# Optimization experiments

Hardware: AMD Instinct MI355X
Metric: run time of the kernel (lower is better)

## Reference

```python
import jax, jax.numpy as jnp
import numpy as np

IN_CHS = 128
NUM_HEADS = 4
WIN = 7
N = WIN * WIN            # 49 tokens per window
QKDIM = 128              # ceil(in_chs/num_groups/num_heads)*num_heads
HEAD_DIM = QKDIM // NUM_HEADS
SCALE = HEAD_DIM ** -0.5
B = 4096                 # batch * num_windows


def _relative_position_index(win_h, win_w):
    coords = np.stack(np.meshgrid(np.arange(win_h), np.arange(win_w), indexing='ij'))  # [2,h,w]
    cf = coords.reshape(2, -1)                      # [2, N]
    rc = (cf[:, :, None] - cf[:, None, :]).transpose(1, 2, 0).astype(np.int64)  # [N,N,2]
    rc[:, :, 0] += win_h - 1
    rc[:, :, 1] += win_w - 1
    rc[:, :, 0] *= 2 * win_w - 1
    return rc.sum(-1)                               # [N, N]


def setup_inputs() -> dict:
    key = jax.random.key(0)
    ks = jax.random.split(key, 8)
    x = jax.random.normal(ks[0], (B, N, IN_CHS), dtype=jnp.float32)
    qk_w = jax.random.normal(ks[1], (2 * QKDIM, IN_CHS), dtype=jnp.float32) * 0.02
    qk_b = jnp.zeros((2 * QKDIM,), dtype=jnp.float32)
    v_w = jax.random.normal(ks[2], (IN_CHS, IN_CHS), dtype=jnp.float32) * 0.02
    v_b = jnp.zeros((IN_CHS,), dtype=jnp.float32)
    proj_w = jax.random.normal(ks[3], (IN_CHS, IN_CHS), dtype=jnp.float32) * 0.02
    proj_b = jnp.zeros((IN_CHS,), dtype=jnp.float32)
    bias_table = jax.random.normal(ks[4], ((2 * WIN - 1) * (2 * WIN - 1), NUM_HEADS), dtype=jnp.float32) * 0.02
    rel_idx = jnp.asarray(_relative_position_index(WIN, WIN))  # [N,N] int64
    return {"x": x, "qk_w": qk_w, "qk_b": qk_b, "v_w": v_w, "v_b": v_b,
            "proj_w": proj_w, "proj_b": proj_b, "bias_table": bias_table,
            "rel_idx": rel_idx}


def reference(x, qk_w, qk_b, v_w, v_b, proj_w, proj_b, bias_table, rel_idx):
    Bn, Nn, C = x.shape
    # fused q/k projection: [B,N,2*qkdim] -> q,k each [B,H,N,d]
    qk = (x @ qk_w.T + qk_b).reshape(Bn, Nn, 2, NUM_HEADS, HEAD_DIM)
    q = qk[:, :, 0].transpose(0, 2, 1, 3)
    k = qk[:, :, 1].transpose(0, 2, 1, 3)
    v = (x @ v_w.T + v_b).reshape(Bn, Nn, NUM_HEADS, -1).transpose(0, 2, 1, 3)
    # windowed QK^T with gathered relative-position bias
    attn = jnp.einsum('bhnd,bhmd->bhnm', q * SCALE, k)
    bias = bias_table[rel_idx.reshape(-1)].reshape(Nn, Nn, NUM_HEADS).transpose(2, 0, 1)
    attn = jax.nn.softmax(attn + bias[None], axis=-1)
    out = jnp.einsum('bhnm,bhmd->bhnd', attn, v).transpose(0, 2, 1, 3).reshape(Bn, Nn, -1)
    return out @ proj_w.T + proj_b
```

## Files before the change

### kernel.cpp

```cpp
#include <hip/hip_runtime.h>
#include <hip/hip_bf16.h>

typedef __attribute__((ext_vector_type(8))) __bf16 bf16x8;
typedef __attribute__((ext_vector_type(4))) short short4v;
typedef __attribute__((ext_vector_type(4))) float f32x4;

#define MFMA(a,b,c) __builtin_amdgcn_mfma_f32_16x16x32_bf16((a),(b),(c),0,0,0)
#define MFMA16(a,b,c) __builtin_amdgcn_mfma_f32_16x16x16bf16_1k((a),(b),(c),0,0,0)

#define XB 0u
#define QB 16384u
#define KB 32768u
#define VT 49152u

static __device__ __forceinline__ unsigned short f2u(float x) {
  return __builtin_bit_cast(unsigned short, static_cast<__bf16>(x));
}
static __device__ __forceinline__ unsigned long long pack4(float a, float b, float c, float d) {
  union { __bf16 h[4]; unsigned long long u; } z;
  z.h[0] = static_cast<__bf16>(a);
  z.h[1] = static_cast<__bf16>(b);
  z.h[2] = static_cast<__bf16>(c);
  z.h[3] = static_cast<__bf16>(d);
  return z.u;
}
static __device__ __forceinline__ unsigned long long pack4v(f32x4 v) {
  return pack4(v[0], v[1], v[2], v[3]);
}
static __device__ __forceinline__ short4v pack4s(float a, float b, float c, float d) {
  union { __bf16 h[4]; short4v s; } z;
  z.h[0] = static_cast<__bf16>(a);
  z.h[1] = static_cast<__bf16>(b);
  z.h[2] = static_cast<__bf16>(c);
  z.h[3] = static_cast<__bf16>(d);
  return z.s;
}
static __device__ __forceinline__ unsigned sw256(unsigned row, unsigned colb) {
  return (row << 8) + (colb ^ ((row & 7u) << 4));
}
static __device__ __forceinline__ unsigned sw128(unsigned row, unsigned colb) {
  return (row << 7) + (colb ^ ((row & 7u) << 4));
}

__global__ void rsa_prep(const float* __restrict__ qk_w, const float* __restrict__ v_w,
                         const float* __restrict__ proj_w, const float* __restrict__ bias_table,
                         unsigned short* __restrict__ wqk, unsigned short* __restrict__ wv,
                         unsigned short* __restrict__ wp, float* __restrict__ biasNN) {
  const float QSCALE = 0.17677669529663687f * 1.4426950408889634f;
  const float LOG2E = 1.4426950408889634f;
  int t = blockIdx.x * blockDim.x + threadIdx.x;
  int stride = gridDim.x * blockDim.x;
  for (int i = t; i < 256 * 128; i += stride) {
    float v = qk_w[i];
    if (i < 128 * 128) v *= QSCALE;
    wqk[i] = f2u(v);
  }
  for (int i = t; i < 128 * 128; i += stride) wv[i] = f2u(v_w[i]);
  for (int i = t; i < 128 * 128; i += stride) wp[i] = f2u(proj_w[i]);
  for (int i = t; i < 4 * 64 * 64; i += stride) {
    int h = i >> 12, r = (i >> 6) & 63, m = i & 63;
    float v = -1e9f;
    if (r < 49 && m < 49) {
      int ri = r / 7, rj = r - ri * 7, mi = m / 7, mj = m - mi * 7;
      int rel = (ri - mi + 6) * 13 + (rj - mj + 6);
      v = bias_table[rel * 4 + h];
    }
    biasNN[i] = v * LOG2E;
  }
}

__global__ __launch_bounds__(256, 2) void rsa_main(
    const float* __restrict__ x, const float* __restrict__ qk_bias,
    const float* __restrict__ v_bias, const float* __restrict__ proj_bias,
    const unsigned short* __restrict__ wqk, const unsigned short* __restrict__ wv,
    const unsigned short* __restrict__ wp, const float* __restrict__ biasNN,
    float* __restrict__ out) {
  __shared__ __align__(16) unsigned char LDS[65536];
  const int tid = threadIdx.x;
  const int w = tid >> 6;
  const int lane = tid & 63;
  const int c = lane & 15;
  const int g = lane >> 4;
  const int b = blockIdx.x;
  const float QBSCALE = 0.17677669529663687f * 1.4426950408889634f;

  {
    const f32x4* xp = reinterpret_cast<const f32x4*>(x + (size_t)b * 6272);
    for (int i = tid; i < 1568; i += 256) {
      f32x4 v = xp[i];
      unsigned row = (unsigned)i >> 5, c4 = (unsigned)i & 31u;
      *reinterpret_cast<unsigned long long*>(LDS + XB + sw256(row, c4 * 8)) = pack4v(v);
    }
    for (int i = tid; i < 480; i += 256) {
      unsigned row = 49 + ((unsigned)i >> 5), c4 = (unsigned)i & 31u;
      *reinterpret_cast<unsigned long long*>(LDS + XB + sw256(row, c4 * 8)) = 0ull;
    }
  }
  __syncthreads();

  __builtin_amdgcn_s_setprio(1);
#pragma unroll
  for (int mi = 0; mi < 4; ++mi) {
    const int mt = (mi < 2) ? (2 * w + mi) : (6 + 2 * w + mi);
    bf16x8 a[4];
    const unsigned short* wrow = wqk + (mt * 16 + c) * 128 + g * 8;
#pragma unroll
    for (int ks = 0; ks < 4; ++ks) a[ks] = *reinterpret_cast<const bf16x8*>(wrow + ks * 32);
    f32x4 bias4 = *reinterpret_cast<const f32x4*>(qk_bias + mt * 16 + g * 4);
    if (mi < 2) { bias4[0] *= QBSCALE; bias4[1] *= QBSCALE; bias4[2] *= QBSCALE; bias4[3] *= QBSCALE; }
    f32x4 acc[4];
#pragma unroll
    for (int nt = 0; nt < 4; ++nt) acc[nt] = bias4;
#pragma unroll
    for (int ks = 0; ks < 4; ++ks) {
#pragma unroll
      for (int nt = 0; nt < 4; ++nt) {
        bf16x8 bf = *reinterpret_cast<const bf16x8*>(LDS + XB + sw256(nt * 16 + c, (ks * 32 + g * 8) * 2));
        acc[nt] = MFMA(a[ks], bf, acc[nt]);
      }
    }
    const unsigned base = (mi < 2) ? QB : KB;
    const unsigned colb = ((mt & 7) * 16 + g * 4) * 2;
#pragma unroll
    for (int nt = 0; nt < 4; ++nt)
      *reinterpret_cast<unsigned long long*>(LDS + base + sw256(nt * 16 + c, colb)) = pack4v(acc[nt]);
  }

#pragma unroll
  for (int ci = 0; ci < 2; ++ci) {
    const int ch = w * 32 + ci * 16 + c;
    const float vb = v_bias[ch];
    bf16x8 bw[4];
    const unsigned short* wrow = wv + ch * 128 + g * 8;
#pragma unroll
    for (int ks = 0; ks < 4; ++ks) bw[ks] = *reinterpret_cast<const bf16x8*>(wrow + ks * 32);
    f32x4 acc[4];
#pragma unroll
    for (int mt = 0; mt < 4; ++mt) acc[mt] = f32x4{vb, vb, vb, vb};
#pragma unroll
    for (int ks = 0; ks < 4; ++ks) {
#pragma unroll
      for (int mt = 0; mt < 4; ++mt) {
        bf16x8 af = *reinterpret_cast<const bf16x8*>(LDS + XB + sw256(mt * 16 + c, (ks * 32 + g * 8) * 2));
        acc[mt] = MFMA(af, bw[ks], acc[mt]);
      }
    }
#pragma unroll
    for (int mt = 0; mt < 4; ++mt)
      *reinterpret_cast<unsigned long long*>(LDS + VT + sw128(ch, (mt * 16 + g * 4) * 2)) =
          pack4v(acc[mt]);
  }
  __builtin_amdgcn_s_setprio(0);

  short4v pk[4][4];
#pragma unroll
  for (int rt = 0; rt < 4; ++rt) {
    f32x4 bbr[4];
    {
      const float* bp = biasNN + ((w * 64 + rt * 16 + c) << 6);
#pragma unroll
      for (int mt = 0; mt < 4; ++mt)
        bbr[mt] = *reinterpret_cast<const f32x4*>(bp + mt * 16 + g * 4);
    }
    bf16x8 qf = *reinterpret_cast<const bf16x8*>(LDS + QB + sw256(rt * 16 + c, w * 64 + g * 16));
    f32x4 s[4];
    __builtin_amdgcn_s_setprio(1);
#pragma unroll
    for (int mt = 0; mt < 4; ++mt) {
      bf16x8 kf = *reinterpret_cast<const bf16x8*>(LDS + KB + sw256(mt * 16 + c, w * 64 + g * 16));
      s[mt] = MFMA(kf, qf, bbr[mt]);
    }
    __builtin_amdgcn_s_setprio(0);
    float v[16];
#pragma unroll
    for (int mt = 0; mt < 4; ++mt) {
#pragma unroll
      for (int j = 0; j < 4; ++j) v[mt * 4 + j] = exp2f(s[mt][j]);
    }
    float p0 = (v[0] + v[1]) + (v[2] + v[3]);
    float p1 = (v[4] + v[5]) + (v[6] + v[7]);
    float p2 = (v[8] + v[9]) + (v[10] + v[11]);
    float p3 = (v[12] + v[13]) + (v[14] + v[15]);
    float sum = (p0 + p1) + (p2 + p3);
    sum += __shfl_xor(sum, 16);
    sum += __shfl_xor(sum, 32);
    const float inv = __builtin_amdgcn_rcpf(sum);
#pragma unroll
    for (int mt = 0; mt < 4; ++mt)
      pk[rt][mt] = pack4s(v[mt * 4] * inv, v[mt * 4 + 1] * inv,
                          v[mt * 4 + 2] * inv, v[mt * 4 + 3] * inv);
  }

  f32x4 od[2][4];
  {
    short4v vfrag[2][4];
#pragma unroll
    for (int ct2 = 0; ct2 < 2; ++ct2)
#pragma unroll
      for (int ks = 0; ks < 4; ++ks)
        vfrag[ct2][ks] = *reinterpret_cast<const short4v*>(
            LDS + VT + sw128((w * 2 + ct2) * 16 + c, (ks * 16 + g * 4) * 2));
#pragma unroll
    for (int ct2 = 0; ct2 < 2; ++ct2)
#pragma unroll
      for (int rt = 0; rt < 4; ++rt) od[ct2][rt] = f32x4{0.f, 0.f, 0.f, 0.f};
    __builtin_amdgcn_s_setprio(1);
#pragma unroll
    for (int ks = 0; ks < 4; ++ks)
#pragma unroll
      for (int ct2 = 0; ct2 < 2; ++ct2)
#pragma unroll
        for (int rt = 0; rt < 4; ++rt)
          od[ct2][rt] = MFMA16(vfrag[ct2][ks], pk[rt][ks], od[ct2][rt]);
    __builtin_amdgcn_s_setprio(0);
  }

#pragma unroll
  for (int ct2 = 0; ct2 < 2; ++ct2)
#pragma unroll
    for (int rt = 0; rt < 4; ++rt) {
      const int r = rt * 16 + c;
      *reinterpret_cast<unsigned long long*>(
          LDS + QB + sw256(r, ((w * 2 + ct2) * 16 + g * 4) * 2)) = pack4v(od[ct2][rt]);
    }
  __syncthreads();

  __builtin_amdgcn_s_setprio(1);
#pragma unroll
  for (int u = 0; u < 2; ++u) {
    const int ct = 2 * w + u;
    bf16x8 ap[4];
    const unsigned short* wrow = wp + (ct * 16 + c) * 128 + g * 8;
#pragma unroll
    for (int ks = 0; ks < 4; ++ks) ap[ks] = *reinterpret_cast<const bf16x8*>(wrow + ks * 32);
    f32x4 pb4 = *reinterpret_cast<const f32x4*>(proj_bias + ct * 16 + g * 4);
    f32x4 acc[4];
#pragma unroll
    for (int nt = 0; nt < 4; ++nt) acc[nt] = pb4;
#pragma unroll
    for (int ks = 0; ks < 4; ++ks) {
#pragma unroll
      for (int nt = 0; nt < 4; ++nt) {
        bf16x8 bf = *reinterpret_cast<const bf16x8*>(LDS + QB + sw256(nt * 16 + c, (ks * 32 + g * 8) * 2));
        acc[nt] = MFMA(ap[ks], bf, acc[nt]);
      }
    }
#pragma unroll
    for (int nt = 0; nt < 4; ++nt) {
      const int tok = nt * 16 + c;
      if (tok < 49) {
        *reinterpret_cast<f32x4*>(out + ((size_t)b * 49 + tok) * 128 + ct * 16 + g * 4) = acc[nt];
      }
    }
  }
  __builtin_amdgcn_s_setprio(0);
}

extern "C" void kernel_launch(void* const* d_in, const int* in_sizes, int n_in,
                              void* d_out, int out_size, void* d_ws, size_t ws_size,
                              hipStream_t stream) {
  const float* x          = (const float*)d_in[0];
  const float* qk_w       = (const float*)d_in[1];
  const float* qk_b       = (const float*)d_in[2];
  const float* v_w        = (const float*)d_in[3];
  const float* v_b        = (const float*)d_in[4];
  const float* proj_w     = (const float*)d_in[5];
  const float* proj_b     = (const float*)d_in[6];
  const float* bias_table = (const float*)d_in[7];
  float* out = (float*)d_out;

  unsigned short* wqk = (unsigned short*)d_ws;
  unsigned short* wv  = wqk + 256 * 128;
  unsigned short* wp  = wv + 128 * 128;
  float* biasNN = (float*)((char*)d_ws + 131072);

  const int B = in_sizes[0] / (49 * 128);

  rsa_prep<<<dim3(128), dim3(512), 0, stream>>>(qk_w, v_w, proj_w, bias_table, wqk, wv, wp, biasNN);
  rsa_main<<<dim3(B), dim3(256), 0, stream>>>(x, qk_b, v_b, proj_b, wqk, wv, wp, biasNN, out);
}
```

Measured before the change: 125.5 us.

## Keep Q/K in registers as MFMA fragments, shrink LDS for three blocks per CU

Q and K projections now stay in registers as bf16 fragments laid out so each wave can feed them straight into the 16x16x16 MFMA for QK^T. This drops the Q and K LDS buffers, shrinking shared memory from 64KB to 48KB, and launch bounds are raised so three blocks can share a CU. Proj weights and bias are loaded before the barrier to hide latency. The risk is higher register pressure at the new occupancy target, which could cause spills.

```diff
diff --git a/kernel.cpp b/kernel.cpp
--- a/kernel.cpp
+++ b/kernel.cpp
@@ -9,9 +9,8 @@
 #define MFMA16(a,b,c) __builtin_amdgcn_mfma_f32_16x16x16bf16_1k((a),(b),(c),0,0,0)
 
 #define XB 0u
-#define QB 16384u
-#define KB 32768u
-#define VT 49152u
+#define VT 16384u
+#define OB 32768u
 
 static __device__ __forceinline__ unsigned short f2u(float x) {
   return __builtin_bit_cast(unsigned short, static_cast<__bf16>(x));
@@ -34,6 +33,9 @@
   z.h[2] = static_cast<__bf16>(c);
   z.h[3] = static_cast<__bf16>(d);
   return z.s;
+}
+static __device__ __forceinline__ short4v pack4sv(f32x4 v) {
+  return pack4s(v[0], v[1], v[2], v[3]);
 }
 static __device__ __forceinline__ unsigned sw256(unsigned row, unsigned colb) {
   return (row << 8) + (colb ^ ((row & 7u) << 4));
@@ -69,13 +71,13 @@
   }
 }
 
-__global__ __launch_bounds__(256, 2) void rsa_main(
+__global__ __launch_bounds__(256, 3) void rsa_main(
     const float* __restrict__ x, const float* __restrict__ qk_bias,
     const float* __restrict__ v_bias, const float* __restrict__ proj_bias,
     const unsigned short* __restrict__ wqk, const unsigned short* __restrict__ wv,
     const unsigned short* __restrict__ wp, const float* __restrict__ biasNN,
     float* __restrict__ out) {
-  __shared__ __align__(16) unsigned char LDS[65536];
+  __shared__ __align__(16) unsigned char LDS[49152];
   const int tid = threadIdx.x;
   const int w = tid >> 6;
   const int lane = tid & 63;
@@ -98,57 +100,64 @@
   }
   __syncthreads();
 
+  f32x4 qacc[2][4], kacc[2][4];
+  {
+#pragma unroll
+    for (int kt = 0; kt < 2; ++kt) {
+      f32x4 qb4 = *reinterpret_cast<const f32x4*>(qk_bias + (2 * w + kt) * 16 + g * 4);
+      qb4[0] *= QBSCALE; qb4[1] *= QBSCALE; qb4[2] *= QBSCALE; qb4[3] *= QBSCALE;
+      f32x4 kb4 = *reinterpret_cast<const f32x4*>(qk_bias + 128 + (2 * w + kt) * 16 + g * 4);
+#pragma unroll
+      for (int nt = 0; nt < 4; ++nt) { qacc[kt][nt] = qb4; kacc[kt][nt] = kb4; }
+    }
+    __builtin_amdgcn_s_setprio(1);
+#pragma unroll
+    for (int ks = 0; ks < 4; ++ks) {
+      bf16x8 wq0 = *reinterpret_cast<const bf16x8*>(wqk + ((2 * w) * 16 + c) * 128 + ks * 32 + g * 8);
+      bf16x8 wq1 = *reinterpret_cast<const bf16x8*>(wqk + ((2 * w + 1) * 16 + c) * 128 + ks * 32 + g * 8);
+      bf16x8 wk0 = *reinterpret_cast<const bf16x8*>(wqk + (128 + (2 * w) * 16 + c) * 128 + ks * 32 + g * 8);
+      bf16x8 wk1 = *reinterpret_cast<const bf16x8*>(wqk + (128 + (2 * w + 1) * 16 + c) * 128 + ks * 32 + g * 8);
+#pragma unroll
+      for (int nt = 0; nt < 4; ++nt) {
+        bf16x8 xf = *reinterpret_cast<const bf16x8*>(LDS + XB + sw256(nt * 16 + c, (ks * 32 + g * 8) * 2));
+        qacc[0][nt] = MFMA(wq0, xf, qacc[0][nt]);
+        qacc[1][nt] = MFMA(wq1, xf, qacc[1][nt]);
+        kacc[0][nt] = MFMA(wk0, xf, kacc[0][nt]);
+        kacc[1][nt] = MFMA(wk1, xf, kacc[1][nt]);
+      }
+    }
+    __builtin_amdgcn_s_setprio(0);
+  }
+  short4v q16[2][4], k16[2][4];
+#pragma unroll
+  for (int kt = 0; kt < 2; ++kt)
+#pragma unroll
+    for (int nt = 0; nt < 4; ++nt) {
+      q16[kt][nt] = pack4sv(qacc[kt][nt]);
+      k16[kt][nt] = pack4sv(kacc[kt][nt]);
+    }
+
   __builtin_amdgcn_s_setprio(1);
 #pragma unroll
-  for (int mi = 0; mi < 4; ++mi) {
-    const int mt = (mi < 2) ? (2 * w + mi) : (6 + 2 * w + mi);
-    bf16x8 a[4];
-    const unsigned short* wrow = wqk + (mt * 16 + c) * 128 + g * 8;
-#pragma unroll
-    for (int ks = 0; ks < 4; ++ks) a[ks] = *reinterpret_cast<const bf16x8*>(wrow + ks * 32);
-    f32x4 bias4 = *reinterpret_cast<const f32x4*>(qk_bias + mt * 16 + g * 4);
-    if (mi < 2) { bias4[0] *= QBSCALE; bias4[1] *= QBSCALE; bias4[2] *= QBSCALE; bias4[3] *= QBSCALE; }
-    f32x4 acc[4];
-#pragma unroll
-    for (int nt = 0; nt < 4; ++nt) acc[nt] = bias4;
+  for (int ci = 0; ci < 2; ++ci) {
+    const int ch = (2 * w + ci) * 16 + c;
+    const float vb = v_bias[ch];
+    f32x4 vacc[4];
+#pragma unroll
+    for (int mt = 0; mt < 4; ++mt) vacc[mt] = f32x4{vb, vb, vb, vb};
 #pragma unroll
     for (int ks = 0; ks < 4; ++ks) {
-#pragma unroll
-      for (int nt = 0; nt < 4; ++nt) {
-        bf16x8 bf = *reinterpret_cast<const bf16x8*>(LDS + XB + sw256(nt * 16 + c, (ks * 32 + g * 8) * 2));
-        acc[nt] = MFMA(a[ks], bf, acc[nt]);
-      }
-    }
-    const unsigned base = (mi < 2) ? QB : KB;
-    const unsigned colb = ((mt & 7) * 16 + g * 4) * 2;
-#pragma unroll
-    for (int nt = 0; nt < 4; ++nt)
-      *reinterpret_cast<unsigned long long*>(LDS + base + sw256(nt * 16 + c, colb)) = pack4v(acc[nt]);
-  }
-
-#pragma unroll
-  for (int ci = 0; ci < 2; ++ci) {
-    const int ch = w * 32 + ci * 16 + c;
-    const float vb = v_bias[ch];
-    bf16x8 bw[4];
-    const unsigned short* wrow = wv + ch * 128 + g * 8;
-#pragma unroll
-    for (int ks = 0; ks < 4; ++ks) bw[ks] = *reinterpret_cast<const bf16x8*>(wrow + ks * 32);
-    f32x4 acc[4];
-#pragma unroll
-    for (int mt = 0; mt < 4; ++mt) acc[mt] = f32x4{vb, vb, vb, vb};
-#pragma unroll
-    for (int ks = 0; ks < 4; ++ks) {
+      bf16x8 bw = *reinterpret_cast<const bf16x8*>(wv + ch * 128 + ks * 32 + g * 8);
 #pragma unroll
       for (int mt = 0; mt < 4; ++mt) {
-        bf16x8 af = *reinterpret_cast<const bf16x8*>(LDS + XB + sw256(mt * 16 + c, (ks * 32 + g * 8) * 2));
-        acc[mt] = MFMA(af, bw[ks], acc[mt]);
+        bf16x8 xf = *reinterpret_cast<const bf16x8*>(LDS + XB + sw256(mt * 16 + c, (ks * 32 + g * 8) * 2));
+        vacc[mt] = MFMA(xf, bw, vacc[mt]);
       }
     }
 #pragma unroll
     for (int mt = 0; mt < 4; ++mt)
       *reinterpret_cast<unsigned long long*>(LDS + VT + sw128(ch, (mt * 16 + g * 4) * 2)) =
-          pack4v(acc[mt]);
+          pack4v(vacc[mt]);
   }
   __builtin_amdgcn_s_setprio(0);
 
@@ -162,14 +171,11 @@
       for (int mt = 0; mt < 4; ++mt)
         bbr[mt] = *reinterpret_cast<const f32x4*>(bp + mt * 16 + g * 4);
     }
-    bf16x8 qf = *reinterpret_cast<const bf16x8*>(LDS + QB + sw256(rt * 16 + c, w * 64 + g * 16));
     f32x4 s[4];
     __builtin_amdgcn_s_setprio(1);
 #pragma unroll
-    for (int mt = 0; mt < 4; ++mt) {
-      bf16x8 kf = *reinterpret_cast<const bf16x8*>(LDS + KB + sw256(mt * 16 + c, w * 64 + g * 16));
-      s[mt] = MFMA(kf, qf, bbr[mt]);
-    }
+    for (int mt = 0; mt < 4; ++mt)
+      s[mt] = MFMA16(k16[1][mt], q16[1][rt], MFMA16(k16[0][mt], q16[0][rt], bbr[mt]));
     __builtin_amdgcn_s_setprio(0);
     float v[16];
 #pragma unroll
@@ -195,61 +201,63 @@
   {
     short4v vfrag[2][4];
 #pragma unroll
-    for (int ct2 = 0; ct2 < 2; ++ct2)
-#pragma unroll
-      for (int ks = 0; ks < 4; ++ks)
-        vfrag[ct2][ks] = *reinterpret_cast<const short4v*>(
-            LDS + VT + sw128((w * 2 + ct2) * 16 + c, (ks * 16 + g * 4) * 2));
-#pragma unroll
-    for (int ct2 = 0; ct2 < 2; ++ct2)
-#pragma unroll
-      for (int rt = 0; rt < 4; ++rt) od[ct2][rt] = f32x4{0.f, 0.f, 0.f, 0.f};
+    for (int ct = 0; ct < 2; ++ct)
+#pragma unroll
+      for (int mt = 0; mt < 4; ++mt)
+        vfrag[ct][mt] = *reinterpret_cast<const short4v*>(
+            LDS + VT + sw128((2 * w + ct) * 16 + c, (mt * 16 + g * 4) * 2));
+#pragma unroll
+    for (int ct = 0; ct < 2; ++ct)
+#pragma unroll
+      for (int rt = 0; rt < 4; ++rt) od[ct][rt] = f32x4{0.f, 0.f, 0.f, 0.f};
     __builtin_amdgcn_s_setprio(1);
 #pragma unroll
-    for (int ks = 0; ks < 4; ++ks)
-#pragma unroll
-      for (int ct2 = 0; ct2 < 2; ++ct2)
+    for (int mt = 0; mt < 4; ++mt)
+#pragma unroll
+      for (int ct = 0; ct < 2; ++ct)
 #pragma unroll
         for (int rt = 0; rt < 4; ++rt)
-          od[ct2][rt] = MFMA16(vfrag[ct2][ks], pk[rt][ks], od[ct2][rt]);
+          od[ct][rt] = MFMA16(vfrag[ct][mt], pk[rt][mt], od[ct][rt]);
     __builtin_amdgcn_s_setprio(0);
   }
 
-#pragma unroll
-  for (int ct2 = 0; ct2 < 2; ++ct2)
-#pragma unroll
-    for (int rt = 0; rt < 4; ++rt) {
-      const int r = rt * 16 + c;
+  bf16x8 ap[2][4];
+  f32x4 pb4[2];
+#pragma unroll
+  for (int u = 0; u < 2; ++u) {
+    const unsigned short* wrow = wp + ((2 * w + u) * 16 + c) * 128 + g * 8;
+#pragma unroll
+    for (int ks = 0; ks < 4; ++ks) ap[u][ks] = *reinterpret_cast<const bf16x8*>(wrow + ks * 32);
+    pb4[u] = *reinterpret_cast<const f32x4*>(proj_bias + (2 * w + u) * 16 + g * 4);
+  }
+
+#pragma unroll
+  for (int ct = 0; ct < 2; ++ct)
+#pragma unroll
+    for (int rt = 0; rt < 4; ++rt)
       *reinterpret_cast<unsigned long long*>(
-          LDS + QB + sw256(r, ((w * 2 + ct2) * 16 + g * 4) * 2)) = pack4v(od[ct2][rt]);
-    }
+          LDS + OB + sw256(rt * 16 + c, ((2 * w + ct) * 16 + g * 4) * 2)) = pack4v(od[ct][rt]);
   __syncthreads();
 
   __builtin_amdgcn_s_setprio(1);
 #pragma unroll
   for (int u = 0; u < 2; ++u) {
-    const int ct = 2 * w + u;
-    bf16x8 ap[4];
-    const unsigned short* wrow = wp + (ct * 16 + c) * 128 + g * 8;
-#pragma unroll
-    for (int ks = 0; ks < 4; ++ks) ap[ks] = *reinterpret_cast<const bf16x8*>(wrow + ks * 32);
-    f32x4 pb4 = *reinterpret_cast<const f32x4*>(proj_bias + ct * 16 + g * 4);
     f32x4 acc[4];
 #pragma unroll
-    for (int nt = 0; nt < 4; ++nt) acc[nt] = pb4;
+    for (int nt = 0; nt < 4; ++nt) acc[nt] = pb4[u];
 #pragma unroll
     for (int ks = 0; ks < 4; ++ks) {
 #pragma unroll
       for (int nt = 0; nt < 4; ++nt) {
-        bf16x8 bf = *reinterpret_cast<const bf16x8*>(LDS + QB + sw256(nt * 16 + c, (ks * 32 + g * 8) * 2));
-        acc[nt] = MFMA(ap[ks], bf, acc[nt]);
+        bf16x8 bf = *reinterpret_cast<const bf16x8*>(LDS + OB + sw256(nt * 16 + c, (ks * 32 + g * 8) * 2));
+        acc[nt] = MFMA(ap[u][ks], bf, acc[nt]);
       }
     }
 #pragma unroll
     for (int nt = 0; nt < 4; ++nt) {
       const int tok = nt * 16 + c;
       if (tok < 49) {
-        *reinterpret_cast<f32x4*>(out + ((size_t)b * 49 + tok) * 128 + ct * 16 + g * 4) = acc[nt];
+        *reinterpret_cast<f32x4*>(out + ((size_t)b * 49 + tok) * 128 + (2 * w + u) * 16 + g * 4) = acc[nt];
       }
     }
   }
```

Measured after the change: 122.3 us. 2.6% less time.
